# Optimization experiments

Measured on AMD Instinct MI355X. Metric: run time of the kernel, lower is better.

Reference implementation:

```python
import jax, jax.numpy as jnp
import numpy as np

NUM_INPUTS = 1024
NUM_HIDDENS = 1024
SIGMA = 0.01


def setup_inputs() -> dict:
    key = jax.random.key(0)
    ks = jax.random.split(key, 7)
    d, h = NUM_INPUTS, NUM_HIDDENS
    w = lambda k, *s: jax.random.normal(k, s, dtype=jnp.float32) * SIGMA
    return {
        "inputs": jax.random.normal(ks[0], (512, 64, d), dtype=jnp.float32),
        "W_xz": w(ks[1], d, h), "W_hz": w(ks[2], h, h), "b_z": jnp.zeros(h, jnp.float32),
        "W_xr": w(ks[3], d, h), "W_hr": w(ks[4], h, h), "b_r": jnp.zeros(h, jnp.float32),
        "W_xh": w(ks[5], d, h), "W_hh": w(ks[6], h, h), "b_h": jnp.zeros(h, jnp.float32),
    }


def reference(inputs, W_xz, W_hz, b_z, W_xr, W_hr, b_r, W_xh, W_hh, b_h):
    T, B, _ = inputs.shape
    H0 = jnp.zeros((B, NUM_HIDDENS), dtype=inputs.dtype)
    # Precompute input projections for all timesteps in one big GEMM each.
    Xz = inputs @ W_xz + b_z  # [T, B, H]
    Xr = inputs @ W_xr + b_r
    Xh = inputs @ W_xh + b_h

    def step(H, xs):
        xz, xr, xh = xs
        Z = jax.nn.sigmoid(xz + H @ W_hz)
        R = jax.nn.sigmoid(xr + H @ W_hr)
        H_tilde = jnp.tanh(xh + (R * H) @ W_hh)
        H_new = Z * H + (1.0 - Z) * H_tilde
        return H_new, H_new

    H_final, outputs = jax.lax.scan(step, H0, (Xz, Xr, Xh))
    return outputs, H_final  # outputs: [T, B, H] (stacked list), H_final: [B, H]
```

## Files before the change

kernel.cpp:

```cpp
#include <hip/hip_runtime.h>
#include <hip/hip_bf16.h>

#define T_STEPS 512
#define BATCH   64
#define HID     1024
#define NBLK    256
#define NSLOT   32
#define SLOT_SH (4 * 16 * 1024)

typedef __attribute__((ext_vector_type(8))) short short8;
typedef __attribute__((ext_vector_type(4))) float f32x4;
typedef __attribute__((ext_vector_type(4))) int  i32x4;

static __device__ __forceinline__ float b2f(unsigned short u){
  union { unsigned u; float f; } c; c.u = ((unsigned)u) << 16; return c.f;
}
static __device__ __forceinline__ unsigned short f2b(float f){
  union { float f; unsigned u; } c; c.f = f;
  unsigned r = c.u + 0x7fffu + ((c.u >> 16) & 1u);
  return (unsigned short)(r >> 16);
}
static __device__ __forceinline__ float sigm(float x){ return 1.0f / (1.0f + __expf(-x)); }
static __device__ __forceinline__ float tanh_fast(float x){ return 2.0f / (1.0f + __expf(-2.0f * x)) - 1.0f; }

#define MFMA __builtin_amdgcn_mfma_f32_16x16x32_bf16

__global__ void gru_init_k(int* __restrict__ flags, int* __restrict__ gready){
  int i = blockIdx.x * blockDim.x + threadIdx.x;
  if (i < 4 * 32 * 32)
    __hip_atomic_store(flags + i, 0, __ATOMIC_RELAXED, __HIP_MEMORY_SCOPE_AGENT);
  if (i < T_STEPS * 32)
    __hip_atomic_store(gready + i, 0, __ATOMIC_RELAXED, __HIP_MEMORY_SCOPE_AGENT);
}

__global__ void gru_prepw_k(const float* __restrict__ w0, const float* __restrict__ w1,
                            const float* __restrict__ w2, const float* __restrict__ w3,
                            const float* __restrict__ w4, const float* __restrict__ w5,
                            unsigned short* __restrict__ wt){
  __shared__ float tile[32][33];
  const float* src;
  switch (blockIdx.z){
    case 0: src = w0; break; case 1: src = w1; break; case 2: src = w2; break;
    case 3: src = w3; break; case 4: src = w4; break; default: src = w5; break;
  }
  int tx = threadIdx.x, ty = threadIdx.y;
  int x0 = blockIdx.x * 32, y0 = blockIdx.y * 32;
  #pragma unroll
  for (int i = 0; i < 32; i += 8)
    tile[ty + i][tx] = src[(size_t)(y0 + ty + i) * HID + x0 + tx];
  __syncthreads();
  unsigned short* dst = wt + (size_t)blockIdx.z * HID * HID;
  #pragma unroll
  for (int i = 0; i < 32; i += 8)
    dst[(size_t)(x0 + ty + i) * HID + y0 + tx] = f2b(tile[tx][ty + i]);
}

static __device__ __forceinline__ void waitflags32(const int* fgrp, int target){
  const int lane = threadIdx.x & 63;
  const int* p = fgrp + (lane & 31) * 32;
  const bool mine = lane < 32;
  for (;;){
    int v = mine ? __hip_atomic_load(p, __ATOMIC_RELAXED, __HIP_MEMORY_SCOPE_AGENT)
                 : 0x7fffffff;
    if (__all(v >= target)) return;
    __builtin_amdgcn_s_sleep(1);
  }
}

static __device__ __forceinline__ void stage_in(const unsigned short* __restrict__ src,
                                                unsigned short* __restrict__ stg, int tid){
  char* sb = (char*)stg;
  const char* sc = (const char*)src;
  #pragma unroll
  for (int c = 0; c < 4; ++c){
    const int b = tid * 16 + c * 8192;
    short8 v = __builtin_nontemporal_load((const short8*)(sc + b));
    *(short8*)(sb + (b ^ (((b >> 11) & 7) << 4))) = v;
  }
}

static __device__ __forceinline__ void pub16(unsigned short* dst, const unsigned short* lds_src){
  i32x4 v = *(const i32x4*)lds_src;
  asm volatile("global_store_dwordx4 %0, %1, off sc0 sc1" :: "v"(dst), "v"(v) : "memory");
}
static __device__ __forceinline__ void pub8(unsigned short* dst, unsigned long long v){
  asm volatile("global_store_dwordx2 %0, %1, off sc0 sc1" :: "v"(dst), "v"(v) : "memory");
}

__global__ __launch_bounds__(512, 1) void gru_main_k(
    const float* __restrict__ inp,
    const unsigned short* __restrict__ wt,
    const float* __restrict__ bz, const float* __restrict__ br, const float* __restrict__ bh,
    unsigned short* __restrict__ G2,
    float* __restrict__ out,
    unsigned short* __restrict__ hb,
    unsigned short* __restrict__ rh,
    int* __restrict__ flags,
    int* __restrict__ gready)
{
  __shared__ __align__(16) char smem[98304];
  const int bid = blockIdx.x;
  const int tid = threadIdx.x;

  if (bid >= 128){
    const int d = bid - 128;
    const int wv = tid >> 6, lane = tid & 63;
    const int l16 = lane & 15, kq = lane >> 4;
    char* sb = (char*)smem;
    const int asw = (l16 & 7) << 4;

    for (int i = 0; i < 24; ++i){
      const int tau = i * 128 + d;
      const int tt = tau / 6, rem = tau % 6, g = rem >> 1, rhh = rem & 1;
      const float* bias_p = (g == 0) ? bz : (g == 1) ? br : bh;

      const float* abase = inp + ((size_t)tt * 64 + rhh * 32) * HID;
      #pragma unroll
      for (int p = 0; p < 16; ++p){
        int e = (p * 512 + tid) * 4;
        float4 v = *(const float4*)(abase + e);
        ushort4 o;
        o.x = f2b(v.x); o.y = f2b(v.y); o.z = f2b(v.z); o.w = f2b(v.w);
        int b = e * 2;
        *(ushort4*)(sb + (b ^ (((b >> 11) & 7) << 4))) = o;
      }
      __syncthreads();

      const int n0 = wv * 128;
      const unsigned short* wslab = wt + (size_t)(2 * g) * HID * HID;
      const unsigned short* wcol[8];
      float bias[8];
      #pragma unroll
      for (int c = 0; c < 8; ++c){
        int n = n0 + c * 16 + l16;
        wcol[c] = wslab + (size_t)n * HID + kq * 8;
        bias[c] = bias_p[n];
      }
      f32x4 acc[2][8];
      #pragma unroll
      for (int r = 0; r < 2; ++r)
        #pragma unroll
        for (int c = 0; c < 8; ++c) acc[r][c] = (f32x4){0.f,0.f,0.f,0.f};

      for (int kk = 0; kk < HID; kk += 32){
        short8 a0 = *(const short8*)(sb + ((l16 * 2048 + kk * 2 + kq * 16) ^ asw));
        short8 a1 = *(const short8*)(sb + (((16 + l16) * 2048 + kk * 2 + kq * 16) ^ asw));
        #pragma unroll
        for (int c = 0; c < 8; ++c){
          short8 bf = *(const short8*)(wcol[c] + kk);
          acc[0][c] = MFMA(a0, bf, acc[0][c], 0, 0, 0);
          acc[1][c] = MFMA(a1, bf, acc[1][c], 0, 0, 0);
        }
      }

      unsigned short* gout = G2 + (((size_t)tt * 3 + g) * 2 + rhh) * 32768;
      #pragma unroll
      for (int c = 0; c < 8; ++c){
        int n = n0 + c * 16 + l16;
        #pragma unroll
        for (int r = 0; r < 2; ++r){
          unsigned lo = (unsigned)f2b(acc[r][c][0] + bias[c]) | ((unsigned)f2b(acc[r][c][1] + bias[c]) << 16);
          unsigned hi = (unsigned)f2b(acc[r][c][2] + bias[c]) | ((unsigned)f2b(acc[r][c][3] + bias[c]) << 16);
          pub8(&gout[(size_t)n * 32 + r * 16 + kq * 4],
               (unsigned long long)lo | ((unsigned long long)hi << 32));
        }
      }
      asm volatile("s_waitcnt vmcnt(0)" ::: "memory");
      __syncthreads();
      if (tid == 0)
        __hip_atomic_fetch_add(gready + tt * 32, 1, __ATOMIC_RELAXED, __HIP_MEMORY_SCOPE_AGENT);
    }
    return;
  }

  unsigned short* stage  = (unsigned short*)smem;
  float*          zlds   = (float*)(smem + 32768);
  float*          hlds   = (float*)(smem + 34880);
  unsigned short* ostage = (unsigned short*)(smem + 36992);

  const int rg  = bid & 3;
  const int cs  = bid >> 2;
  const int w    = tid >> 6;
  const int lane = tid & 63;
  const int l16  = lane & 15;
  const int kq   = lane >> 4;

  const int myct = (w < 4) ? (w & 1) : ((w < 6) ? (w - 4) : 0);
  const int col  = cs * 32 + myct * 16 + l16;
  const int gA   = (w >> 1) & 1;
  const int erow0 = kq * 4;
  const int ecol  = myct * 16 + l16;

  short8 wreg[32];
  if (w < 6){
    const int slot = (w < 2) ? 1 : (w < 4) ? 3 : 5;
    const unsigned short* p = wt + (size_t)slot * HID * HID + (size_t)col * HID + kq * 8;
    #pragma unroll
    for (int i = 0; i < 32; ++i) wreg[i] = *(const short8*)(p + i * 32);
  }

  int* fgrp   = flags + rg * 32 * 32;
  int* myflag = fgrp + cs * 32;

  for (int i = tid; i < 16 * 33; i += 512) hlds[i] = 0.f;
  __syncthreads();

  const int asw = (l16 & 7) << 4;
  const int abase = l16 * 2048 + kq * 16;
  const int pidx = tid - 448;
  const int prow = pidx >> 2, pc8 = (pidx & 3) * 8;

  const size_t g2rh = (size_t)(rg >> 1) * 32768;
  const int    g2r  = (rg & 1) * 16 + erow0;

  for (int t = 0; t < T_STEPS; ++t){
    unsigned short* hb_w = hb + (size_t)(t & (NSLOT - 1)) * SLOT_SH + rg * 16384;
    unsigned short* rh_w = rh + (size_t)(t & (NSLOT - 1)) * SLOT_SH + rg * 16384;
    const unsigned short* hb_r = hb + (size_t)((t - 1) & (NSLOT - 1)) * SLOT_SH + rg * 16384;

    unsigned long long gx = 0;
    if (w < 6){
      const int* gp = gready + t * 32;
      int v = (lane == 0) ? __hip_atomic_load(gp, __ATOMIC_RELAXED, __HIP_MEMORY_SCOPE_AGENT) : 6;
      while (!__all(v >= 6)){
        __builtin_amdgcn_s_sleep(2);
        v = (lane == 0) ? __hip_atomic_load(gp, __ATOMIC_RELAXED, __HIP_MEMORY_SCOPE_AGENT) : 6;
      }
      const int gate = (w < 4) ? gA : 2;
      gx = __hip_atomic_load((const unsigned long long*)
             (G2 + ((size_t)t * 3 + gate) * 65536 + g2rh + (size_t)col * 32 + g2r),
             __ATOMIC_RELAXED, __HIP_MEMORY_SCOPE_AGENT);
    }

    if (t){
      if (w == 0) waitflags32(fgrp, 2 * t);
      __syncthreads();
      stage_in(hb_r, stage, tid);
      __syncthreads();
    }
    if (w < 4){
      f32x4 a0 = {0.f,0.f,0.f,0.f}, a1 = {0.f,0.f,0.f,0.f};
      if (t){
        const char* sb = (const char*)stage;
        #pragma unroll
        for (int i = 0; i < 32; i += 2){
          short8 f0 = *(const short8*)(sb + ((abase + i * 64) ^ asw));
          short8 f1 = *(const short8*)(sb + ((abase + i * 64 + 64) ^ asw));
          a0 = MFMA(f0, wreg[i],     a0, 0, 0, 0);
          a1 = MFMA(f1, wreg[i + 1], a1, 0, 0, 0);
        }
      }
      #pragma unroll
      for (int j = 0; j < 4; ++j){
        float g = sigm(a0[j] + a1[j] + b2f((unsigned short)(gx >> (16 * j))));
        if (w < 2) zlds[(erow0 + j) * 33 + ecol] = g;
        else       ostage[(erow0 + j) * 32 + ecol] =
                     f2b(g * hlds[(erow0 + j) * 33 + ecol]);
      }
    }
    __syncthreads();

    if (t){
      if (tid >= 448) pub16(rh_w + prow * 1024 + cs * 32 + pc8, &ostage[prow * 32 + pc8]);
      if (tid == 448){
        asm volatile("s_waitcnt vmcnt(0)" ::: "memory");
        __hip_atomic_store(myflag, 2 * t + 1, __ATOMIC_RELAXED, __HIP_MEMORY_SCOPE_AGENT);
      }
      if (w == 0) waitflags32(fgrp, 2 * t + 1);
      __syncthreads();
      stage_in(rh_w, stage, tid);
      __syncthreads();
    }

    float hn[4];
    if (w == 4 || w == 5){
      f32x4 a0 = {0.f,0.f,0.f,0.f}, a1 = {0.f,0.f,0.f,0.f};
      if (t){
        const char* sb = (const char*)stage;
        #pragma unroll
        for (int i = 0; i < 32; i += 2){
          short8 f0 = *(const short8*)(sb + ((abase + i * 64) ^ asw));
          short8 f1 = *(const short8*)(sb + ((abase + i * 64 + 64) ^ asw));
          a0 = MFMA(f0, wreg[i],     a0, 0, 0, 0);
          a1 = MFMA(f1, wreg[i + 1], a1, 0, 0, 0);
        }
      }
      #pragma unroll
      for (int j = 0; j < 4; ++j){
        int i33 = (erow0 + j) * 33 + ecol;
        float ht = tanh_fast(a0[j] + a1[j] + b2f((unsigned short)(gx >> (16 * j))));
        float z  = zlds[i33], hp = hlds[i33];
        hn[j] = z * hp + (1.0f - z) * ht;
        hlds[i33] = hn[j];
        ostage[(erow0 + j) * 32 + ecol] = f2b(hn[j]);
      }
    }
    __syncthreads();
    if (t < T_STEPS - 1){
      if (tid >= 448) pub16(hb_w + prow * 1024 + cs * 32 + pc8, &ostage[prow * 32 + pc8]);
      if (tid == 448){
        asm volatile("s_waitcnt vmcnt(0)" ::: "memory");
        __hip_atomic_store(myflag, 2 * t + 2, __ATOMIC_RELAXED, __HIP_MEMORY_SCOPE_AGENT);
      }
    }
    if (w == 4 || w == 5){
      #pragma unroll
      for (int j = 0; j < 4; ++j){
        __builtin_nontemporal_store(hn[j],
            &out[((size_t)t * BATCH + rg * 16 + erow0 + j) * HID + col]);
        if (t == T_STEPS - 1)
          __builtin_nontemporal_store(hn[j],
              &out[(size_t)T_STEPS * BATCH * HID + (size_t)(rg * 16 + erow0 + j) * HID + col]);
      }
    }
  }
}

extern "C" void kernel_launch(void* const* d_in, const int* in_sizes, int n_in,
                              void* d_out, int out_size, void* d_ws, size_t ws_size,
                              hipStream_t stream){
  const float* inputs = (const float*)d_in[0];
  const float* W_xz = (const float*)d_in[1];
  const float* W_hz = (const float*)d_in[2];
  const float* b_z  = (const float*)d_in[3];
  const float* W_xr = (const float*)d_in[4];
  const float* W_hr = (const float*)d_in[5];
  const float* b_r  = (const float*)d_in[6];
  const float* W_xh = (const float*)d_in[7];
  const float* W_hh = (const float*)d_in[8];
  const float* b_h  = (const float*)d_in[9];
  float* out = (float*)d_out;

  char* ws = (char*)d_ws;
  int*            flags  = (int*)ws;
  int*            gready = (int*)(ws + 16384);
  unsigned short* hb     = (unsigned short*)(ws + 81920);
  unsigned short* rh     = (unsigned short*)(ws + 81920 + 4194304);
  unsigned short* wt     = (unsigned short*)(ws + 81920 + 8388608);
  unsigned short* G2     = (unsigned short*)(ws + 81920 + 8388608 + 12582912);

  gru_init_k<<<64, 256, 0, stream>>>(flags, gready);
  gru_prepw_k<<<dim3(32, 32, 6), dim3(32, 8), 0, stream>>>(W_xz, W_hz, W_xr, W_hr, W_xh, W_hh, wt);
  gru_main_k<<<NBLK, 512, 0, stream>>>(inputs, wt, b_z, b_r, b_h, G2, out, hb, rh, flags, gready);
}
```

Measured before the change: 3.019 ms.

## Read recurrent state directly from global memory instead of staging through LDS

Removes the LDS staging of the hidden-state and R*H slices. Each compute wave now polls the group flags itself and loads its MFMA A-fragments straight from global memory. This drops two block-wide barriers and a staging copy per half-step, so only the waves that need the data wait on the flags. Publishing is moved to wave 7 alone, with separate output staging buffers for R*H and H. In exchange, every wave issues its own global loads and its own flag polling, and the hidden state is re-read from L2 by each wave rather than shared once through LDS.

Result: slower. 6.293 ms (+108.5%).

```diff
diff --git a/kernel.cpp b/kernel.cpp
--- a/kernel.cpp
+++ b/kernel.cpp
@@ -64,18 +64,6 @@
                  : 0x7fffffff;
     if (__all(v >= target)) return;
     __builtin_amdgcn_s_sleep(1);
-  }
-}
-
-static __device__ __forceinline__ void stage_in(const unsigned short* __restrict__ src,
-                                                unsigned short* __restrict__ stg, int tid){
-  char* sb = (char*)stg;
-  const char* sc = (const char*)src;
-  #pragma unroll
-  for (int c = 0; c < 4; ++c){
-    const int b = tid * 16 + c * 8192;
-    short8 v = __builtin_nontemporal_load((const short8*)(sc + b));
-    *(short8*)(sb + (b ^ (((b >> 11) & 7) << 4))) = v;
   }
 }
 
@@ -173,10 +161,10 @@
     return;
   }
 
-  unsigned short* stage  = (unsigned short*)smem;
-  float*          zlds   = (float*)(smem + 32768);
-  float*          hlds   = (float*)(smem + 34880);
-  unsigned short* ostage = (unsigned short*)(smem + 36992);
+  float*          zlds    = (float*)smem;
+  float*          hlds    = (float*)(smem + 2112);
+  unsigned short* ostageR = (unsigned short*)(smem + 4224);
+  unsigned short* ostageH = (unsigned short*)(smem + 5248);
 
   const int rg  = bid & 3;
   const int cs  = bid >> 2;
@@ -185,7 +173,7 @@
   const int l16  = lane & 15;
   const int kq   = lane >> 4;
 
-  const int myct = (w < 4) ? (w & 1) : ((w < 6) ? (w - 4) : 0);
+  const int myct = w & 1;
   const int col  = cs * 32 + myct * 16 + l16;
   const int gA   = (w >> 1) & 1;
   const int erow0 = kq * 4;
@@ -205,10 +193,8 @@
   for (int i = tid; i < 16 * 33; i += 512) hlds[i] = 0.f;
   __syncthreads();
 
-  const int asw = (l16 & 7) << 4;
-  const int abase = l16 * 2048 + kq * 16;
-  const int pidx = tid - 448;
-  const int prow = pidx >> 2, pc8 = (pidx & 3) * 8;
+  const int afo = l16 * 1024 + kq * 8;
+  const int prow = lane >> 2, pc8 = (lane & 3) * 8;
 
   const size_t g2rh = (size_t)(rg >> 1) * 32768;
   const int    g2r  = (rg & 1) * 16 + erow0;
@@ -232,20 +218,15 @@
              __ATOMIC_RELAXED, __HIP_MEMORY_SCOPE_AGENT);
     }
 
-    if (t){
-      if (w == 0) waitflags32(fgrp, 2 * t);
-      __syncthreads();
-      stage_in(hb_r, stage, tid);
-      __syncthreads();
-    }
     if (w < 4){
       f32x4 a0 = {0.f,0.f,0.f,0.f}, a1 = {0.f,0.f,0.f,0.f};
       if (t){
-        const char* sb = (const char*)stage;
+        waitflags32(fgrp, 2 * t);
+        const unsigned short* ap = hb_r + afo;
         #pragma unroll
         for (int i = 0; i < 32; i += 2){
-          short8 f0 = *(const short8*)(sb + ((abase + i * 64) ^ asw));
-          short8 f1 = *(const short8*)(sb + ((abase + i * 64 + 64) ^ asw));
+          short8 f0 = *(const short8*)(ap + i * 32);
+          short8 f1 = *(const short8*)(ap + i * 32 + 32);
           a0 = MFMA(f0, wreg[i],     a0, 0, 0, 0);
           a1 = MFMA(f1, wreg[i + 1], a1, 0, 0, 0);
         }
@@ -254,33 +235,30 @@
       for (int j = 0; j < 4; ++j){
         float g = sigm(a0[j] + a1[j] + b2f((unsigned short)(gx >> (16 * j))));
         if (w < 2) zlds[(erow0 + j) * 33 + ecol] = g;
-        else       ostage[(erow0 + j) * 32 + ecol] =
+        else       ostageR[(erow0 + j) * 32 + ecol] =
                      f2b(g * hlds[(erow0 + j) * 33 + ecol]);
       }
     }
     __syncthreads();
 
-    if (t){
-      if (tid >= 448) pub16(rh_w + prow * 1024 + cs * 32 + pc8, &ostage[prow * 32 + pc8]);
-      if (tid == 448){
+    if (t && w == 7){
+      pub16(rh_w + prow * 1024 + cs * 32 + pc8, &ostageR[lane * 8]);
+      if (lane == 0){
         asm volatile("s_waitcnt vmcnt(0)" ::: "memory");
         __hip_atomic_store(myflag, 2 * t + 1, __ATOMIC_RELAXED, __HIP_MEMORY_SCOPE_AGENT);
       }
-      if (w == 0) waitflags32(fgrp, 2 * t + 1);
-      __syncthreads();
-      stage_in(rh_w, stage, tid);
-      __syncthreads();
     }
 
     float hn[4];
     if (w == 4 || w == 5){
       f32x4 a0 = {0.f,0.f,0.f,0.f}, a1 = {0.f,0.f,0.f,0.f};
       if (t){
-        const char* sb = (const char*)stage;
+        waitflags32(fgrp, 2 * t + 1);
+        const unsigned short* ap = rh_w + afo;
         #pragma unroll
         for (int i = 0; i < 32; i += 2){
-          short8 f0 = *(const short8*)(sb + ((abase + i * 64) ^ asw));
-          short8 f1 = *(const short8*)(sb + ((abase + i * 64 + 64) ^ asw));
+          short8 f0 = *(const short8*)(ap + i * 32);
+          short8 f1 = *(const short8*)(ap + i * 32 + 32);
           a0 = MFMA(f0, wreg[i],     a0, 0, 0, 0);
           a1 = MFMA(f1, wreg[i + 1], a1, 0, 0, 0);
         }
@@ -292,13 +270,14 @@
         float z  = zlds[i33], hp = hlds[i33];
         hn[j] = z * hp + (1.0f - z) * ht;
         hlds[i33] = hn[j];
-        ostage[(erow0 + j) * 32 + ecol] = f2b(hn[j]);
+        ostageH[(erow0 + j) * 32 + ecol] = f2b(hn[j]);
       }
     }
     __syncthreads();
-    if (t < T_STEPS - 1){
-      if (tid >= 448) pub16(hb_w + prow * 1024 + cs * 32 + pc8, &ostage[prow * 32 + pc8]);
-      if (tid == 448){
+
+    if (t < T_STEPS - 1 && w == 7){
+      pub16(hb_w + prow * 1024 + cs * 32 + pc8, &ostageH[lane * 8]);
+      if (lane == 0){
         asm volatile("s_waitcnt vmcnt(0)" ::: "memory");
         __hip_atomic_store(myflag, 2 * t + 2, __ATOMIC_RELAXED, __HIP_MEMORY_SCOPE_AGENT);
       }
```
